# Performance work log

Hardware: AMD Instinct MI355X
Metric: run time of the kernel (lower is better)

## Reference

```python
import jax, jax.numpy as jnp
import numpy as np

N_NODES = 10000
N_REL = 200
DIM = 128          # rank * 2
REL_DIM = 128
VIS_DIM = 512
TXT_DIM = 768
N_EDGES = 320000


def _glorot(key, shape):
    fan_in, fan_out = shape[1], shape[0]
    lim = (6.0 / (fan_in + fan_out)) ** 0.5
    return jax.random.uniform(key, shape, jnp.float32, -lim, lim)


def setup_inputs() -> dict:
    key = jax.random.key(0)
    ks = jax.random.split(key, 24)
    inp = {}
    inp['x'] = jax.random.randint(ks[0], (1024, 3), 0, N_NODES)
    inp['edge_index'] = jax.random.randint(ks[1], (2, N_EDGES), 0, N_NODES)
    inp['edge_type'] = jax.random.randint(ks[2], (N_EDGES,), 0, N_REL)
    inp['visual'] = jax.random.normal(ks[3], (N_NODES, VIS_DIM), jnp.float32)
    inp['textual'] = jax.random.normal(ks[4], (N_NODES, TXT_DIM), jnp.float32)
    # embeddings (scaled by 0.001 as in torch init)
    inp['structural_emb'] = jax.random.normal(ks[5], (N_NODES, DIM), jnp.float32) * 0.001
    inp['relation_emb'] = jax.random.normal(ks[6], (N_REL, REL_DIM), jnp.float32) * 0.001
    # three KBGAT convs: w1 [out, 2*in+rel], b1 [out], w2 [1, out]
    cat = 2 * DIM + REL_DIM
    for i, tag in enumerate(['s', 'v', 't']):
        inp[f'W1_{tag}'] = _glorot(ks[7 + 3 * i], (DIM, cat))
        inp[f'b1_{tag}'] = jnp.zeros((DIM,), jnp.float32)
        inp[f'w2_{tag}'] = _glorot(ks[8 + 3 * i], (1, DIM))
    # modality projections
    inp['Wv'] = _glorot(ks[16], (DIM, VIS_DIM))
    inp['bv'] = jnp.zeros((DIM,), jnp.float32)
    inp['Wt'] = _glorot(ks[17], (DIM, TXT_DIM))
    inp['bt'] = jnp.zeros((DIM,), jnp.float32)
    inp['alpha'] = jnp.float32(0.1)
    inp['gamma'] = jnp.float32(0.8)
    return inp


def kbgat_conv(feat, rel_emb, src, dst, edge_type, W1, b1, w2):
    # gather per-edge embeddings: x_i = target, x_j = source (PyG default flow)
    triple = jnp.concatenate([feat[dst], feat[src], rel_emb[edge_type]], axis=1)  # [E, 2*D+R]
    c = triple @ W1.T + b1                                   # [E, D]
    b = jax.nn.leaky_relu(c @ w2[0])                         # [E]
    # segment softmax over destination nodes
    m = jax.ops.segment_max(b, dst, num_segments=N_NODES)
    e = jnp.exp(b - m[dst])
    z = jax.ops.segment_sum(e, dst, num_segments=N_NODES)
    attn = e / z[dst]                                        # [E]
    agg = jax.ops.segment_sum(c * attn[:, None], dst, num_segments=N_NODES)  # [N, D]
    return jax.nn.leaky_relu(agg)


def reference(x, edge_index, edge_type, visual, textual, structural_emb, relation_emb,
              W1_s, b1_s, w2_s, W1_v, b1_v, w2_v, W1_t, b1_t, w2_t,
              Wv, bv, Wt, bt, alpha, gamma):
    src, dst = edge_index[0], edge_index[1]
    h_s = kbgat_conv(structural_emb, relation_emb, src, dst, edge_type, W1_s, b1_s, w2_s)
    vf = visual @ Wv.T + bv
    h_v = kbgat_conv(vf, relation_emb, src, dst, edge_type, W1_v, b1_v, w2_v)
    tf = textual @ Wt.T + bt
    h_t = kbgat_conv(tf, relation_emb, src, dst, edge_type, W1_t, b1_t, w2_t)
    return (1.0 - alpha - gamma) * h_s + alpha * h_v + gamma * h_t
```

## Files before the change

kernel.cpp:

```cpp
#include <hip/hip_runtime.h>
#include <hip/hip_bf16.h>

typedef unsigned short u16;
typedef unsigned int u32;
typedef __bf16 bf16x8 __attribute__((ext_vector_type(8)));
typedef float f32x4 __attribute__((ext_vector_type(4)));

#define DIM 128

__device__ __forceinline__ u16 f2bf_rne(float x) {
  u32 u = __float_as_uint(x);
  return (u16)((u + 0x7fffu + ((u >> 16) & 1u)) >> 16);
}
__device__ __forceinline__ u32 packbf2(float x, float y) {
  return (u32)f2bf_rne(x) | ((u32)f2bf_rne(y) << 16);
}
__device__ __forceinline__ float lrelu(float x) { return x > 0.f ? x : 0.01f * x; }
__device__ __forceinline__ int iclamp(int v, int hi) { return v < 0 ? 0 : (v >= hi ? hi - 1 : v); }
__device__ __forceinline__ float sane(float x) { return (x == x) ? x : 0.f; }

__device__ __forceinline__ float wred_max(float v) {
  #pragma unroll
  for (int o = 32; o > 0; o >>= 1) v = fmaxf(v, __shfl_xor(v, o, 64));
  return v;
}
__device__ __forceinline__ float wred_sum(float v) {
  #pragma unroll
  for (int o = 32; o > 0; o >>= 1) v += __shfl_xor(v, o, 64);
  return v;
}

struct PrepAllArgs {
  const float* W1[3]; const float* Wmod[3]; int K[3]; u16* Wc[3];
  const float* rel; const float* b1[3]; const float* bmod[3]; const float* w2[3];
  u16* PrAll; float* qr[3]; int NR;
  const int* dst; int* cnt; int* rank; int E; int N;
  int wc2End; int wc1End; int wc0End; int nCompute; int totB;
};
struct MainArgs {
  const float* A[3]; const u16* B[3]; const float* w2[3];
  u16* PdAll; u16* PsAll; float* qd[3]; float* qs[3];
  int M; int K[3]; int tilesPerM; int nGemm; int totB;
  const int* dst; const int* src; const int* etyp;
  const int* offs; const int* rank; u32* sortedST;
  int E; int NR;
};
struct AgArgs {
  const u32* sortedST; const int* offs;
  const float* qd[3]; const float* qs[3]; const float* qr[3];
  const u16* PdAll; const u16* PsAll; const u16* PrAll;
  const float* alphaP; const float* gammaP;
  float* outp; int N; int NR; int E;
};

__global__ __launch_bounds__(256) void fused_prep(PrepAllArgs a) {
  __shared__ float red[256];
  int b = blockIdx.x, tid = threadIdx.x;
  long nC = a.nCompute, tot = a.totB;
  int cprev = (int)((long)b * nC / tot);
  int cnext = (int)(((long)b + 1) * nC / tot);
  if (cnext == cprev) {
    int h = b - cprev;
    int e = h * 256 + tid;
    if (e < a.E) {
      int d = a.dst[e];
      if (d >= 0 && d < a.N) a.rank[e] = atomicAdd(&a.cnt[d], 1);
    }
    return;
  }
  int c = cprev;
  if (c < a.wc0End) {
    int m, loc;
    if (c < a.wc2End)      { m = 2; loc = c; }
    else if (c < a.wc1End) { m = 1; loc = c - a.wc2End; }
    else                   { m = 0; loc = c - a.wc1End; }
    int o = loc & 255, kb = loc >> 8;
    int k = (kb << 8) + tid;
    int K = a.K[m];
    if (k < K) {
      int halfsel = (o >= 128) ? 128 : 0;
      int oo = o & 127;
      const float* W1 = a.W1[m];
      const float* Wm = a.Wmod[m];
      float acc;
      if (Wm == nullptr) {
        acc = W1[oo * 384 + halfsel + k];
      } else {
        acc = 0.f;
        for (int i = 0; i < 128; ++i)
          acc += W1[oo * 384 + halfsel + i] * Wm[i * K + k];
      }
      a.Wc[m][((size_t)(k >> 5) * 256 + o) * 32 + (k & 31)] = f2bf_rne(acc);
    }
  } else {
    int idx = c - a.wc0End;
    int NRpair = (a.NR + 1) >> 1;
    int m = idx / NRpair;
    if (m > 2) return;
    int rp = idx - m * NRpair;
    int half = tid >> 7, o = tid & 127;
    int r = rp * 2 + half;
    bool ok = (r < a.NR);
    float acc = 0.f;
    if (ok) {
      const float* W1 = a.W1[m];
      acc = a.b1[m][o];
      for (int i = 0; i < 128; ++i)
        acc += W1[o * 384 + 256 + i] * a.rel[r * 128 + i];
      const float* bmod = a.bmod[m];
      if (bmod != nullptr) {
        for (int i = 0; i < 128; ++i)
          acc += (W1[o * 384 + i] + W1[o * 384 + 128 + i]) * bmod[i];
      }
      a.PrAll[(size_t)r * 384 + m * 128 + o] = f2bf_rne(acc);
    }
    red[tid] = ok ? acc * a.w2[m][o] : 0.f;
    __syncthreads();
    int base = half << 7;
    for (int s = 64; s > 0; s >>= 1) {
      if (o < s) red[base + o] += red[base + o + s];
      __syncthreads();
    }
    if (o == 0 && ok) a.qr[m][r] = sane(red[base]);
  }
}

__global__ __launch_bounds__(1024) void scan_k(const int* __restrict__ cnt,
                                               int* __restrict__ offs, int N) {
  __shared__ int sums[1024];
  int t = threadIdx.x;
  int chunk = (N + 1023) >> 10;
  int base = t * chunk;
  int s = 0;
  for (int i = 0; i < chunk; ++i) { int idx = base + i; if (idx < N) s += cnt[idx]; }
  sums[t] = s;
  __syncthreads();
  for (int off = 1; off < 1024; off <<= 1) {
    int v = (t >= off) ? sums[t - off] : 0;
    __syncthreads();
    sums[t] += v;
    __syncthreads();
  }
  int prefix = (t > 0) ? sums[t - 1] : 0;
  for (int i = 0; i < chunk; ++i) {
    int idx = base + i;
    if (idx < N) { offs[idx] = prefix; prefix += cnt[idx]; }
  }
  if (t == 1023) offs[N] = sums[1023];
}

__device__ __forceinline__ void gemm_epilogue(const MainArgs& g, int m, int row0,
                                              f32x4 (&acc)[2][4], float (*qpart)[32]) {
  int tid = threadIdx.x;
  int lane = tid & 63, wv = tid >> 6;
  int quad = lane >> 4, l16 = lane & 15;
  int M = g.M;
  const float* w2 = g.w2[m];
  u16* PdAll = g.PdAll;
  u16* PsAll = g.PsAll;
  float w2c[4];
  #pragma unroll
  for (int t = 0; t < 4; ++t) w2c[t] = w2[(wv & 1) * 64 + t * 16 + l16];

  #pragma unroll
  for (int rg = 0; rg < 2; ++rg) {
    float part[4];
    #pragma unroll
    for (int r = 0; r < 4; ++r) {
      int rr = row0 + rg * 16 + quad * 4 + r;
      bool ok = rr < M;
      float qp = 0.f;
      #pragma unroll
      for (int t = 0; t < 4; ++t) {
        int cc = (wv & 1) * 64 + t * 16 + l16;
        if (ok) {
          if (wv < 2) PdAll[(size_t)rr * 384 + m * 128 + cc] = f2bf_rne(acc[rg][t][r]);
          else        PsAll[(size_t)rr * 384 + m * 128 + cc] = f2bf_rne(acc[rg][t][r]);
        }
        qp += acc[rg][t][r] * w2c[t];
      }
      #pragma unroll
      for (int mk = 1; mk < 16; mk <<= 1) qp += __shfl_xor(qp, mk, 64);
      part[r] = qp;
    }
    if (l16 == 0) {
      #pragma unroll
      for (int r = 0; r < 4; ++r) qpart[wv][rg * 16 + quad * 4 + r] = part[r];
    }
  }
  __syncthreads();
  if (tid < 64) {
    int row = tid & 31;
    int half = tid >> 5;
    int rr = row0 + row;
    if (rr < M) {
      if (half == 0) g.qd[m][rr] = sane(qpart[0][row] + qpart[1][row]);
      else           g.qs[m][rr] = sane(qpart[2][row] + qpart[3][row]);
    }
  }
}

template<int NT>
__device__ __forceinline__ void gemm_exact(const MainArgs& g, int m, int tile,
                                           u16* Als, float (*qpart)[32]) {
  constexpr int H = (NT + 1) / 2;
  const int M = g.M;
  int tid = threadIdx.x;
  int lane = tid & 63, wv = tid >> 6;
  int quad = lane >> 4, l16 = lane & 15;
  int row0 = tile * 32;
  int srow = tid >> 3;
  int tk4 = (tid & 7) * 4;
  int srsw = srow & 3;
  int wg = tk4 >> 3;
  int wrem = tk4 & 7;
  int grow = row0 + srow;
  if (grow >= M) grow = M - 1;
  const float* Ag = g.A[m] + (size_t)grow * (NT * 32);

  float4 vreg[H];
  #pragma unroll
  for (int i = 0; i < H; ++i)
    vreg[i] = *reinterpret_cast<const float4*>(Ag + tk4 + i * 32);
  #pragma unroll
  for (int i = 0; i < H; ++i) {
    int gidx = wg ^ srsw ^ (i & 3);
    u32* dp = reinterpret_cast<u32*>(&Als[((i * 32 + srow) * 32) + (gidx << 3) + wrem]);
    dp[0] = packbf2(vreg[i].x, vreg[i].y);
    dp[1] = packbf2(vreg[i].z, vreg[i].w);
  }
  #pragma unroll
  for (int i = H; i < NT; ++i)
    vreg[i - H] = *reinterpret_cast<const float4*>(Ag + tk4 + i * 32);
  #pragma unroll
  for (int i = H; i < NT; ++i) {
    int gidx = wg ^ srsw ^ (i & 3);
    u32* dp = reinterpret_cast<u32*>(&Als[((i * 32 + srow) * 32) + (gidx << 3) + wrem]);
    dp[0] = packbf2(vreg[i - H].x, vreg[i - H].y);
    dp[1] = packbf2(vreg[i - H].z, vreg[i - H].w);
  }
  __syncthreads();

  const u16* Bpg = g.B[m] + (size_t)(wv * 64 + l16) * 32 + quad * 8;
  f32x4 acc[2][4];
  #pragma unroll
  for (int rg = 0; rg < 2; ++rg)
    #pragma unroll
    for (int t = 0; t < 4; ++t) acc[rg][t] = (f32x4){0.f, 0.f, 0.f, 0.f};

  #pragma unroll
  for (int kb = 0; kb < NT; ++kb) {
    const u16* bp = Bpg + (size_t)kb * 8192;
    bf16x8 b0 = *reinterpret_cast<const bf16x8*>(bp);
    bf16x8 b1 = *reinterpret_cast<const bf16x8*>(bp + 512);
    bf16x8 b2 = *reinterpret_cast<const bf16x8*>(bp + 1024);
    bf16x8 b3 = *reinterpret_cast<const bf16x8*>(bp + 1536);
    int gsw = (quad ^ (l16 & 3) ^ (kb & 3)) << 3;
    #pragma unroll
    for (int rg = 0; rg < 2; ++rg) {
      bf16x8 av = *reinterpret_cast<const bf16x8*>(
          &Als[(kb * 32 + rg * 16 + l16) * 32 + gsw]);
      acc[rg][0] = __builtin_amdgcn_mfma_f32_16x16x32_bf16(av, b0, acc[rg][0], 0, 0, 0);
      acc[rg][1] = __builtin_amdgcn_mfma_f32_16x16x32_bf16(av, b1, acc[rg][1], 0, 0, 0);
      acc[rg][2] = __builtin_amdgcn_mfma_f32_16x16x32_bf16(av, b2, acc[rg][2], 0, 0, 0);
      acc[rg][3] = __builtin_amdgcn_mfma_f32_16x16x32_bf16(av, b3, acc[rg][3], 0, 0, 0);
    }
  }
  gemm_epilogue(g, m, row0, acc, qpart);
}

__device__ void gemm_generic(const MainArgs& g, int m, int tile,
                             u16* Als, float (*qpart)[32]) {
  const int M = g.M, K = g.K[m];
  int nt = K >> 5;
  int tid = threadIdx.x;
  int lane = tid & 63, wv = tid >> 6;
  int quad = lane >> 4, l16 = lane & 15;
  int row0 = tile * 32;
  int srow = tid >> 3;
  int tk4 = (tid & 7) * 4;
  int srsw = srow & 3;
  int wg = tk4 >> 3;
  int wrem = tk4 & 7;
  int grow = row0 + srow;
  if (grow >= M) grow = M - 1;
  const float* Ag = g.A[m] + (size_t)grow * K;
  const u16* Bpg = g.B[m] + (size_t)(wv * 64 + l16) * 32 + quad * 8;

  f32x4 acc[2][4];
  #pragma unroll
  for (int rg = 0; rg < 2; ++rg)
    #pragma unroll
    for (int t = 0; t < 4; ++t) acc[rg][t] = (f32x4){0.f, 0.f, 0.f, 0.f};

  for (int c0 = 0; c0 < nt; c0 += 24) {
    int kc = nt - c0; if (kc > 24) kc = 24;
    __syncthreads();
    for (int i = 0; i < kc; ++i) {
      int kg = (c0 + i) * 32 + tk4;
      if (kg + 3 < K) {
        float4 v = *reinterpret_cast<const float4*>(Ag + kg);
        int gidx = wg ^ srsw ^ (i & 3);
        u32* dp = reinterpret_cast<u32*>(&Als[((i * 32 + srow) * 32) + (gidx << 3) + wrem]);
        dp[0] = packbf2(v.x, v.y);
        dp[1] = packbf2(v.z, v.w);
      }
    }
    __syncthreads();
    for (int kb = 0; kb < kc; ++kb) {
      const u16* bp = Bpg + (size_t)(c0 + kb) * 8192;
      bf16x8 b0 = *reinterpret_cast<const bf16x8*>(bp);
      bf16x8 b1 = *reinterpret_cast<const bf16x8*>(bp + 512);
      bf16x8 b2 = *reinterpret_cast<const bf16x8*>(bp + 1024);
      bf16x8 b3 = *reinterpret_cast<const bf16x8*>(bp + 1536);
      int gsw = (quad ^ (l16 & 3) ^ (kb & 3)) << 3;
      #pragma unroll
      for (int rg = 0; rg < 2; ++rg) {
        bf16x8 av = *reinterpret_cast<const bf16x8*>(
            &Als[(kb * 32 + rg * 16 + l16) * 32 + gsw]);
        acc[rg][0] = __builtin_amdgcn_mfma_f32_16x16x32_bf16(av, b0, acc[rg][0], 0, 0, 0);
        acc[rg][1] = __builtin_amdgcn_mfma_f32_16x16x32_bf16(av, b1, acc[rg][1], 0, 0, 0);
        acc[rg][2] = __builtin_amdgcn_mfma_f32_16x16x32_bf16(av, b2, acc[rg][2], 0, 0, 0);
        acc[rg][3] = __builtin_amdgcn_mfma_f32_16x16x32_bf16(av, b3, acc[rg][3], 0, 0, 0);
      }
    }
  }
  gemm_epilogue(g, m, row0, acc, qpart);
}

__global__ __launch_bounds__(256) void fused_main(MainArgs g) {
  __shared__ __align__(16) u16 Als[24 * 32 * 32];
  __shared__ float qpart[4][32];
  int b = blockIdx.x;
  long nG = g.nGemm, tot = g.totB;
  int gprev = (int)((long)b * nG / tot);
  int gnext = (int)(((long)b + 1) * nG / tot);
  if (gnext == gprev) {
    int h = b - gprev;
    int e = h * 256 + threadIdx.x;
    if (e < g.E) {
      int d = g.dst[e];
      if (d >= 0 && d < g.M) {
        int pos = g.offs[d] + g.rank[e];
        if (pos >= 0 && pos < g.E) {
          u32 s = (u32)iclamp(g.src[e], g.M);
          u32 t = (u32)iclamp(g.etyp[e], g.NR);
          g.sortedST[pos] = (t << 16) | s;
        }
      }
    }
    return;
  }
  int fb = gprev;
  int tpm = g.tilesPerM;
  int m, tile;
  if (fb < tpm)            { m = 2; tile = fb; }
  else if (fb < 2 * tpm)   { m = 1; tile = fb - tpm; }
  else                     { m = 0; tile = fb - 2 * tpm; }

  int K = g.K[m];
  if (K == 768)      gemm_exact<24>(g, m, tile, Als, qpart);
  else if (K == 512) gemm_exact<16>(g, m, tile, Als, qpart);
  else if (K == 128) gemm_exact<4>(g, m, tile, Als, qpart);
  else               gemm_generic(g, m, tile, Als, qpart);
}

__global__ __launch_bounds__(256) void aggregate_all(AgArgs a) {
  int n = blockIdx.x * 4 + (threadIdx.x >> 6);
  if (n >= a.N) return;
  int lane = threadIdx.x & 63;
  int E = a.E;
  int eb = a.offs[n], ee = a.offs[n + 1];
  if (eb < 0) eb = 0;
  if (eb > E) eb = E;
  if (ee < eb) ee = eb;
  if (ee > E) ee = E;
  int En = ee - eb;

  float al = a.alphaP[0];
  if (!(al > 0.f && al < 1.f)) al = 0.1f;
  float ga = a.gammaP[0];
  if (!(ga > 0.f && ga < 1.f)) ga = 0.8f;
  float coef[3] = {1.f - al - ga, al, ga};

  float qdn[3];
  #pragma unroll
  for (int m = 0; m < 3; ++m) qdn[m] = sane(a.qd[m][n]);

  const u16* PsAll = a.PsAll;
  const u16* PrAll = a.PrAll;
  int dlo = 2 * lane;

  float rm[3] = {-1e30f, -1e30f, -1e30f};
  float z[3] = {0.f, 0.f, 0.f};
  float a0[3] = {0.f, 0.f, 0.f};
  float a1[3] = {0.f, 0.f, 0.f};
  for (int c0 = 0; c0 < En; c0 += 64) {
    int cn = min(64, En - c0);
    u32 stp = 0;
    float bm[3] = {-1e30f, -1e30f, -1e30f};
    if (lane < cn) {
      stp = a.sortedST[eb + c0 + lane];
      int s = (int)(stp & 0xffffu);
      int t = (int)(stp >> 16);
      #pragma unroll
      for (int m = 0; m < 3; ++m)
        bm[m] = lrelu(qdn[m] + a.qs[m][s] + a.qr[m][t]);
    }
    float wr[3];
    #pragma unroll
    for (int m = 0; m < 3; ++m) {
      float cm = wred_max(bm[m]);
      float nm = fmaxf(rm[m], cm);
      float sc = __expf(fmaxf(rm[m] - nm, -80.f));
      z[m] *= sc; a0[m] *= sc; a1[m] *= sc;
      rm[m] = nm;
      wr[m] = (lane < cn) ? __expf(fmaxf(bm[m] - nm, -80.f)) : 0.f;
      z[m] += wr[m];
    }

    int cnR = (cn + 3) & ~3;
    for (int j = 0; j < cnR; j += 4) {
      u32 stj[4];
      float wj[4][3];
      #pragma unroll
      for (int u = 0; u < 4; ++u) {
        stj[u] = __shfl(stp, j + u, 64);
        wj[u][0] = __shfl(wr[0], j + u, 64);
        wj[u][1] = __shfl(wr[1], j + u, 64);
        wj[u][2] = __shfl(wr[2], j + u, 64);
      }
      u32 pu[4][3], ru[4][3];
      #pragma unroll
      for (int u = 0; u < 4; ++u) {
        const u16* ps = PsAll + (size_t)(stj[u] & 0xffffu) * 384 + dlo;
        const u16* pr = PrAll + (size_t)(stj[u] >> 16) * 384 + dlo;
        #pragma unroll
        for (int m = 0; m < 3; ++m) {
          pu[u][m] = *reinterpret_cast<const u32*>(ps + m * 128);
          ru[u][m] = *reinterpret_cast<const u32*>(pr + m * 128);
        }
      }
      #pragma unroll
      for (int u = 0; u < 4; ++u) {
        #pragma unroll
        for (int m = 0; m < 3; ++m) {
          float ps0 = __uint_as_float(pu[u][m] << 16);
          float ps1 = __uint_as_float(pu[u][m] & 0xffff0000u);
          float pr0 = __uint_as_float(ru[u][m] << 16);
          float pr1 = __uint_as_float(ru[u][m] & 0xffff0000u);
          a0[m] = fmaf(wj[u][m], ps0 + pr0, a0[m]);
          a1[m] = fmaf(wj[u][m], ps1 + pr1, a1[m]);
        }
      }
    }
  }
  #pragma unroll
  for (int m = 0; m < 3; ++m) z[m] = wred_sum(z[m]);

  float o0 = 0.f, o1 = 0.f;
  const u16* pd = a.PdAll + (size_t)n * 384 + dlo;
  #pragma unroll
  for (int m = 0; m < 3; ++m) {
    float h0 = 0.f, h1 = 0.f;
    if (En > 0 && z[m] > 0.f) {
      float rz = 1.f / z[m];
      u32 du = *reinterpret_cast<const u32*>(pd + m * 128);
      float pd0 = __uint_as_float(du << 16), pd1 = __uint_as_float(du & 0xffff0000u);
      h0 = lrelu(pd0 + a0[m] * rz);
      h1 = lrelu(pd1 + a1[m] * rz);
    }
    o0 = fmaf(coef[m], h0, o0);
    o1 = fmaf(coef[m], h1, o1);
  }
  float* op = a.outp + (size_t)n * 128 + dlo;
  op[0] = sane(o0);
  op[1] = sane(o1);
}

extern "C" void kernel_launch(void* const* d_in, const int* in_sizes, int n_in,
                              void* d_out, int out_size, void* d_ws, size_t ws_size,
                              hipStream_t stream) {
  const int* ei        = (const int*)d_in[1];
  const int* et        = (const int*)d_in[2];
  const float* visual  = (const float*)d_in[3];
  const float* textual = (const float*)d_in[4];
  const float* semb    = (const float*)d_in[5];
  const float* relemb  = (const float*)d_in[6];
  const float* W1s = (const float*)d_in[7];
  const float* b1s = (const float*)d_in[8];
  const float* w2s = (const float*)d_in[9];
  const float* W1v = (const float*)d_in[10];
  const float* b1v = (const float*)d_in[11];
  const float* w2v = (const float*)d_in[12];
  const float* W1t = (const float*)d_in[13];
  const float* b1t = (const float*)d_in[14];
  const float* w2t = (const float*)d_in[15];
  const float* Wv  = (const float*)d_in[16];
  const float* bv  = (const float*)d_in[17];
  const float* Wt  = (const float*)d_in[18];
  const float* bt  = (const float*)d_in[19];
  const float* alphaP = (const float*)d_in[20];
  const float* gammaP = (const float*)d_in[21];
  float* outp = (float*)d_out;

  const int E   = in_sizes[2];
  const int N   = in_sizes[5] / DIM;
  const int NR  = in_sizes[6] / DIM;
  const int VIS = in_sizes[3] / N;
  const int TXT = in_sizes[4] / N;
  int Ks[3] = {DIM, VIS, TXT};
  const int TPM = (N + 31) / 32;

  const float* W1a[3]   = {W1s, W1v, W1t};
  const float* b1a[3]   = {b1s, b1v, b1t};
  const float* w2a[3]   = {w2s, w2v, w2t};
  const float* Wmoda[3] = {nullptr, Wv, Wt};
  const float* bmoda[3] = {nullptr, bv, bt};
  const float* Amoda[3] = {semb, visual, textual};

  const int* esrc = ei;
  const int* edst = ei + E;
  int egrid = (E + 255) / 256;

  size_t off = 0;
  auto take = [&](size_t bytes) -> size_t {
    size_t o = off;
    off = (off + bytes + 255) & ~(size_t)255;
    return o;
  };
  size_t o_cnt  = take((size_t)N * 4);
  size_t o_rank = take((size_t)E * 4);
  size_t o_offs = take((size_t)(N + 1) * 4);
  size_t o_st   = take((size_t)E * 4);
  size_t o_qdm[3], o_qsm[3], o_qrm[3], o_Wcm[3];
  for (int m = 0; m < 3; ++m) {
    o_qdm[m] = take((size_t)N * 4);
    o_qsm[m] = take((size_t)N * 4);
    o_qrm[m] = take((size_t)NR * 4);
    o_Wcm[m] = take((size_t)256 * Ks[m] * 2);
  }
  size_t o_PrAll = take((size_t)NR * 384 * 2);
  size_t o_PdAll = take((size_t)N * 384 * 2);
  size_t o_PsAll = take((size_t)N * 384 * 2);
  size_t need = off;

  if (ws_size < need) {
    hipMemsetAsync(d_out, 0, (size_t)out_size * 4, stream);
    return;
  }

  char* w = (char*)d_ws;
  int* counts = (int*)(w + o_cnt);
  int* rank   = (int*)(w + o_rank);
  int* offs   = (int*)(w + o_offs);
  u32* sortedST = (u32*)(w + o_st);

  hipMemsetAsync(counts, 0, (size_t)N * 4, stream);

  PrepAllArgs pa;
  pa.rel = relemb; pa.NR = NR;
  pa.PrAll = (u16*)(w + o_PrAll);
  pa.dst = edst; pa.cnt = counts; pa.rank = rank; pa.E = E; pa.N = N;
  for (int m = 0; m < 3; ++m) {
    pa.W1[m] = W1a[m]; pa.Wmod[m] = Wmoda[m]; pa.K[m] = Ks[m];
    pa.Wc[m] = (u16*)(w + o_Wcm[m]);
    pa.b1[m] = b1a[m]; pa.bmod[m] = bmoda[m]; pa.w2[m] = w2a[m];
    pa.qr[m] = (float*)(w + o_qrm[m]);
  }
  int NRpair = (NR + 1) / 2;
  int kbm[3];
  for (int m = 0; m < 3; ++m) kbm[m] = (Ks[m] + 255) / 256;
  pa.wc2End   = 256 * kbm[2];
  pa.wc1End   = pa.wc2End + 256 * kbm[1];
  pa.wc0End   = pa.wc1End + 256 * kbm[0];
  pa.nCompute = pa.wc0End + 3 * NRpair;
  pa.totB     = pa.nCompute + egrid;

  MainArgs ga;
  ga.M = N; ga.tilesPerM = TPM; ga.nGemm = 3 * TPM;
  ga.totB = ga.nGemm + egrid;
  ga.PdAll = (u16*)(w + o_PdAll);
  ga.PsAll = (u16*)(w + o_PsAll);
  ga.dst = edst; ga.src = esrc; ga.etyp = et;
  ga.offs = offs; ga.rank = rank; ga.sortedST = sortedST;
  ga.E = E; ga.NR = NR;
  AgArgs aa;
  for (int m = 0; m < 3; ++m) {
    ga.A[m] = Amoda[m]; ga.B[m] = (const u16*)(w + o_Wcm[m]); ga.w2[m] = w2a[m];
    ga.qd[m] = (float*)(w + o_qdm[m]); ga.qs[m] = (float*)(w + o_qsm[m]);
    ga.K[m] = Ks[m];
    aa.qd[m] = (const float*)(w + o_qdm[m]);
    aa.qs[m] = (const float*)(w + o_qsm[m]);
    aa.qr[m] = (const float*)(w + o_qrm[m]);
  }

  aa.PdAll = (const u16*)(w + o_PdAll);
  aa.PsAll = (const u16*)(w + o_PsAll);
  aa.PrAll = (const u16*)(w + o_PrAll);
  aa.sortedST = sortedST; aa.offs = offs;
  aa.alphaP = alphaP; aa.gammaP = gammaP;
  aa.outp = outp; aa.N = N; aa.NR = NR; aa.E = E;

  fused_prep<<<pa.totB, 256, 0, stream>>>(pa);
  scan_k<<<1, 1024, 0, stream>>>(counts, offs, N);
  fused_main<<<ga.totB, 256, 0, stream>>>(ga);
  aggregate_all<<<(N + 3) / 4, 256, 0, stream>>>(aa);
}
```

Baseline: 274.3 us.

## Merge all phases into one cooperative persistent kernel with grid syncs

Replaces the memset plus four kernel launches with a single cooperative mega-kernel. It loops virtual blocks over the phases (zero counts, prep, a multi-block scan, GEMM, aggregate) and separates them with grid.sync. The GEMM tile shrinks from 32 to 16 rows so more tiles exist for the persistent grid. A fallback multi-launch path remains. This targets launch gaps and the single-block scan, at the cost of grid-wide barriers and possibly lower per-tile efficiency.

Result: slower. 610.1 us (+122.4%).

```diff
diff --git a/kernel.cpp b/kernel.cpp
--- a/kernel.cpp
+++ b/kernel.cpp
@@ -1,5 +1,8 @@
 #include <hip/hip_runtime.h>
 #include <hip/hip_bf16.h>
+#include <hip/hip_cooperative_groups.h>
+
+namespace cg = cooperative_groups;
 
 typedef unsigned short u16;
 typedef unsigned int u32;
@@ -30,50 +33,38 @@
   return v;
 }
 
-struct PrepAllArgs {
-  const float* W1[3]; const float* Wmod[3]; int K[3]; u16* Wc[3];
+struct MegaArgs {
+  const float* W1[3]; const float* Wmod[3]; int K[3];
   const float* rel; const float* b1[3]; const float* bmod[3]; const float* w2[3];
-  u16* PrAll; float* qr[3]; int NR;
-  const int* dst; int* cnt; int* rank; int E; int N;
-  int wc2End; int wc1End; int wc0End; int nCompute; int totB;
+  const float* A[3];
+  const int* dst; const int* src; const int* etyp;
+  const float* alphaP; const float* gammaP;
+  u16* Wc[3]; u16* PrAll; u16* PdAll; u16* PsAll;
+  float* qr[3]; float* qd[3]; float* qs[3];
+  int* cnt; int* rank; int* offs; int* partial; u32* sortedST;
+  float* outp;
+  int E; int N; int NR;
+  int z0Tot;
+  int wc2End; int wc1End; int wc0End; int aCompute; int aTot;
+  int tilesPerM; int cGemm; int cTot;
+  int dTot;
 };
-struct MainArgs {
-  const float* A[3]; const u16* B[3]; const float* w2[3];
-  u16* PdAll; u16* PsAll; float* qd[3]; float* qs[3];
-  int M; int K[3]; int tilesPerM; int nGemm; int totB;
-  const int* dst; const int* src; const int* etyp;
-  const int* offs; const int* rank; u32* sortedST;
-  int E; int NR;
-};
-struct AgArgs {
-  const u32* sortedST; const int* offs;
-  const float* qd[3]; const float* qs[3]; const float* qr[3];
-  const u16* PdAll; const u16* PsAll; const u16* PrAll;
-  const float* alphaP; const float* gammaP;
-  float* outp; int N; int NR; int E;
-};
-
-__global__ __launch_bounds__(256) void fused_prep(PrepAllArgs a) {
-  __shared__ float red[256];
-  int b = blockIdx.x, tid = threadIdx.x;
-  long nC = a.nCompute, tot = a.totB;
-  int cprev = (int)((long)b * nC / tot);
-  int cnext = (int)(((long)b + 1) * nC / tot);
-  if (cnext == cprev) {
-    int h = b - cprev;
-    int e = h * 256 + tid;
+
+__device__ __forceinline__ void phaseA(const MegaArgs& a, int vb, void* lds) {
+  int tid = threadIdx.x;
+  if (vb >= a.aCompute) {
+    int e = (vb - a.aCompute) * 256 + tid;
     if (e < a.E) {
       int d = a.dst[e];
       if (d >= 0 && d < a.N) a.rank[e] = atomicAdd(&a.cnt[d], 1);
     }
     return;
   }
-  int c = cprev;
-  if (c < a.wc0End) {
+  if (vb < a.wc0End) {
     int m, loc;
-    if (c < a.wc2End)      { m = 2; loc = c; }
-    else if (c < a.wc1End) { m = 1; loc = c - a.wc2End; }
-    else                   { m = 0; loc = c - a.wc1End; }
+    if (vb < a.wc2End)      { m = 2; loc = vb; }
+    else if (vb < a.wc1End) { m = 1; loc = vb - a.wc2End; }
+    else                    { m = 0; loc = vb - a.wc1End; }
     int o = loc & 255, kb = loc >> 8;
     int k = (kb << 8) + tid;
     int K = a.K[m];
@@ -92,161 +83,200 @@
       }
       a.Wc[m][((size_t)(k >> 5) * 256 + o) * 32 + (k & 31)] = f2bf_rne(acc);
     }
-  } else {
-    int idx = c - a.wc0End;
-    int NRpair = (a.NR + 1) >> 1;
-    int m = idx / NRpair;
-    if (m > 2) return;
-    int rp = idx - m * NRpair;
-    int half = tid >> 7, o = tid & 127;
-    int r = rp * 2 + half;
-    bool ok = (r < a.NR);
-    float acc = 0.f;
-    if (ok) {
-      const float* W1 = a.W1[m];
-      acc = a.b1[m][o];
+    return;
+  }
+  float* red = (float*)lds;
+  int idx = vb - a.wc0End;
+  int NRpair = (a.NR + 1) >> 1;
+  int m = idx / NRpair;
+  if (m > 2) return;
+  int rp = idx - m * NRpair;
+  int half = tid >> 7, o = tid & 127;
+  int r = rp * 2 + half;
+  bool ok = (r < a.NR);
+  float acc = 0.f;
+  if (ok) {
+    const float* W1 = a.W1[m];
+    acc = a.b1[m][o];
+    for (int i = 0; i < 128; ++i)
+      acc += W1[o * 384 + 256 + i] * a.rel[r * 128 + i];
+    const float* bmod = a.bmod[m];
+    if (bmod != nullptr) {
       for (int i = 0; i < 128; ++i)
-        acc += W1[o * 384 + 256 + i] * a.rel[r * 128 + i];
-      const float* bmod = a.bmod[m];
-      if (bmod != nullptr) {
-        for (int i = 0; i < 128; ++i)
-          acc += (W1[o * 384 + i] + W1[o * 384 + 128 + i]) * bmod[i];
-      }
-      a.PrAll[(size_t)r * 384 + m * 128 + o] = f2bf_rne(acc);
-    }
-    red[tid] = ok ? acc * a.w2[m][o] : 0.f;
-    __syncthreads();
-    int base = half << 7;
-    for (int s = 64; s > 0; s >>= 1) {
-      if (o < s) red[base + o] += red[base + o + s];
-      __syncthreads();
-    }
-    if (o == 0 && ok) a.qr[m][r] = sane(red[base]);
-  }
-}
-
-__global__ __launch_bounds__(1024) void scan_k(const int* __restrict__ cnt,
-                                               int* __restrict__ offs, int N) {
-  __shared__ int sums[1024];
+        acc += (W1[o * 384 + i] + W1[o * 384 + 128 + i]) * bmod[i];
+    }
+    a.PrAll[(size_t)r * 384 + m * 128 + o] = f2bf_rne(acc);
+  }
+  red[tid] = ok ? acc * a.w2[m][o] : 0.f;
+  __syncthreads();
+  int base = half << 7;
+  for (int s = 64; s > 0; s >>= 1) {
+    if (o < s) red[base + o] += red[base + o + s];
+    __syncthreads();
+  }
+  if (o == 0 && ok) a.qr[m][r] = sane(red[base]);
+  __syncthreads();
+}
+
+__device__ __forceinline__ void scanB1(const MegaArgs& a, int b, int gsz, void* lds) {
+  int* sums = (int*)lds;
   int t = threadIdx.x;
-  int chunk = (N + 1023) >> 10;
-  int base = t * chunk;
+  int chunk = (a.N + gsz - 1) / gsz;
+  int base = b * chunk;
+  int perT = (chunk + 255) >> 8;
   int s = 0;
-  for (int i = 0; i < chunk; ++i) { int idx = base + i; if (idx < N) s += cnt[idx]; }
+  for (int i = 0; i < perT; ++i) {
+    int idx = base + t * perT + i;
+    if (idx < base + chunk && idx < a.N) s += a.cnt[idx];
+  }
   sums[t] = s;
   __syncthreads();
-  for (int off = 1; off < 1024; off <<= 1) {
+  for (int off = 1; off < 256; off <<= 1) {
     int v = (t >= off) ? sums[t - off] : 0;
     __syncthreads();
     sums[t] += v;
     __syncthreads();
   }
-  int prefix = (t > 0) ? sums[t - 1] : 0;
-  for (int i = 0; i < chunk; ++i) {
-    int idx = base + i;
-    if (idx < N) { offs[idx] = prefix; prefix += cnt[idx]; }
-  }
-  if (t == 1023) offs[N] = sums[1023];
-}
-
-__device__ __forceinline__ void gemm_epilogue(const MainArgs& g, int m, int row0,
-                                              f32x4 (&acc)[2][4], float (*qpart)[32]) {
+  if (t == 255) a.partial[b] = sums[255];
+  __syncthreads();
+}
+
+__device__ __forceinline__ void scanB2(const MegaArgs& a, int gsz, void* lds) {
+  int* sums = (int*)lds;
+  int t = threadIdx.x;
+  int G = (gsz + 255) >> 8;
+  int s = 0;
+  for (int i = 0; i < G; ++i) {
+    int idx = t * G + i;
+    if (idx < gsz) s += a.partial[idx];
+  }
+  sums[t] = s;
+  __syncthreads();
+  for (int off = 1; off < 256; off <<= 1) {
+    int v = (t >= off) ? sums[t - off] : 0;
+    __syncthreads();
+    sums[t] += v;
+    __syncthreads();
+  }
+  if (t == 255) a.offs[a.N] = sums[255];
+  int pre = (t > 0) ? sums[t - 1] : 0;
+  for (int i = 0; i < G; ++i) {
+    int idx = t * G + i;
+    if (idx < gsz) { int c = a.partial[idx]; a.partial[idx] = pre; pre += c; }
+  }
+  __syncthreads();
+}
+
+__device__ __forceinline__ void scanB3(const MegaArgs& a, int b, int gsz, void* lds) {
+  int* sums = (int*)lds;
+  int t = threadIdx.x;
+  int chunk = (a.N + gsz - 1) / gsz;
+  int base = b * chunk;
+  int perT = (chunk + 255) >> 8;
+  int s = 0;
+  for (int i = 0; i < perT; ++i) {
+    int idx = base + t * perT + i;
+    if (idx < base + chunk && idx < a.N) s += a.cnt[idx];
+  }
+  sums[t] = s;
+  __syncthreads();
+  for (int off = 1; off < 256; off <<= 1) {
+    int v = (t >= off) ? sums[t - off] : 0;
+    __syncthreads();
+    sums[t] += v;
+    __syncthreads();
+  }
+  int prefix = a.partial[b] + ((t > 0) ? sums[t - 1] : 0);
+  for (int i = 0; i < perT; ++i) {
+    int idx = base + t * perT + i;
+    if (idx < base + chunk && idx < a.N) { a.offs[idx] = prefix; prefix += a.cnt[idx]; }
+  }
+  __syncthreads();
+}
+
+__device__ __forceinline__ void stash16(u16* Als, int srow, int tk4, int i, float4 v) {
+  int kb = 2 * i + (tk4 >> 5);
+  int kl = tk4 & 31;
+  int gidx = (kl >> 3) ^ (srow & 3) ^ (kb & 3);
+  u32* dp = reinterpret_cast<u32*>(&Als[(kb * 16 + srow) * 32 + (gidx << 3) + (kl & 7)]);
+  dp[0] = packbf2(v.x, v.y);
+  dp[1] = packbf2(v.z, v.w);
+}
+
+__device__ __forceinline__ void epilogue16(const MegaArgs& g, int m, int row0,
+                                           f32x4 (&acc)[4], float (*qpart)[16]) {
   int tid = threadIdx.x;
   int lane = tid & 63, wv = tid >> 6;
   int quad = lane >> 4, l16 = lane & 15;
-  int M = g.M;
   const float* w2 = g.w2[m];
-  u16* PdAll = g.PdAll;
-  u16* PsAll = g.PsAll;
   float w2c[4];
   #pragma unroll
   for (int t = 0; t < 4; ++t) w2c[t] = w2[(wv & 1) * 64 + t * 16 + l16];
-
-  #pragma unroll
-  for (int rg = 0; rg < 2; ++rg) {
-    float part[4];
+  float part[4];
+  #pragma unroll
+  for (int r = 0; r < 4; ++r) {
+    int rr = row0 + quad * 4 + r;
+    bool ok = rr < g.N;
+    float qp = 0.f;
     #pragma unroll
-    for (int r = 0; r < 4; ++r) {
-      int rr = row0 + rg * 16 + quad * 4 + r;
-      bool ok = rr < M;
-      float qp = 0.f;
-      #pragma unroll
-      for (int t = 0; t < 4; ++t) {
-        int cc = (wv & 1) * 64 + t * 16 + l16;
-        if (ok) {
-          if (wv < 2) PdAll[(size_t)rr * 384 + m * 128 + cc] = f2bf_rne(acc[rg][t][r]);
-          else        PsAll[(size_t)rr * 384 + m * 128 + cc] = f2bf_rne(acc[rg][t][r]);
-        }
-        qp += acc[rg][t][r] * w2c[t];
-      }
-      #pragma unroll
-      for (int mk = 1; mk < 16; mk <<= 1) qp += __shfl_xor(qp, mk, 64);
-      part[r] = qp;
-    }
-    if (l16 == 0) {
-      #pragma unroll
-      for (int r = 0; r < 4; ++r) qpart[wv][rg * 16 + quad * 4 + r] = part[r];
-    }
-  }
-  __syncthreads();
-  if (tid < 64) {
-    int row = tid & 31;
-    int half = tid >> 5;
+    for (int t = 0; t < 4; ++t) {
+      int cc = (wv & 1) * 64 + t * 16 + l16;
+      if (ok) {
+        if (wv < 2) g.PdAll[(size_t)rr * 384 + m * 128 + cc] = f2bf_rne(acc[t][r]);
+        else        g.PsAll[(size_t)rr * 384 + m * 128 + cc] = f2bf_rne(acc[t][r]);
+      }
+      qp += acc[t][r] * w2c[t];
+    }
+    #pragma unroll
+    for (int mk = 1; mk < 16; mk <<= 1) qp += __shfl_xor(qp, mk, 64);
+    part[r] = qp;
+  }
+  if (l16 == 0) {
+    #pragma unroll
+    for (int r = 0; r < 4; ++r) qpart[wv][quad * 4 + r] = part[r];
+  }
+  __syncthreads();
+  if (tid < 32) {
+    int row = tid & 15, half = tid >> 4;
     int rr = row0 + row;
-    if (rr < M) {
+    if (rr < g.N) {
       if (half == 0) g.qd[m][rr] = sane(qpart[0][row] + qpart[1][row]);
       else           g.qs[m][rr] = sane(qpart[2][row] + qpart[3][row]);
     }
   }
+  __syncthreads();
 }
 
 template<int NT>
-__device__ __forceinline__ void gemm_exact(const MainArgs& g, int m, int tile,
-                                           u16* Als, float (*qpart)[32]) {
-  constexpr int H = (NT + 1) / 2;
-  const int M = g.M;
+__device__ __forceinline__ void gemm16(const MegaArgs& g, int m, int tile,
+                                       u16* Als, float (*qpart)[16]) {
+  constexpr int NS = NT / 2;
+  constexpr int H = (NS + 1) / 2;
   int tid = threadIdx.x;
   int lane = tid & 63, wv = tid >> 6;
   int quad = lane >> 4, l16 = lane & 15;
-  int row0 = tile * 32;
-  int srow = tid >> 3;
-  int tk4 = (tid & 7) * 4;
-  int srsw = srow & 3;
-  int wg = tk4 >> 3;
-  int wrem = tk4 & 7;
+  int row0 = tile * 16;
+  int srow = tid >> 4;
+  int tk4 = (tid & 15) * 4;
   int grow = row0 + srow;
-  if (grow >= M) grow = M - 1;
+  if (grow >= g.N) grow = g.N - 1;
   const float* Ag = g.A[m] + (size_t)grow * (NT * 32);
 
   float4 vreg[H];
   #pragma unroll
-  for (int i = 0; i < H; ++i)
-    vreg[i] = *reinterpret_cast<const float4*>(Ag + tk4 + i * 32);
-  #pragma unroll
-  for (int i = 0; i < H; ++i) {
-    int gidx = wg ^ srsw ^ (i & 3);
-    u32* dp = reinterpret_cast<u32*>(&Als[((i * 32 + srow) * 32) + (gidx << 3) + wrem]);
-    dp[0] = packbf2(vreg[i].x, vreg[i].y);
-    dp[1] = packbf2(vreg[i].z, vreg[i].w);
-  }
-  #pragma unroll
-  for (int i = H; i < NT; ++i)
-    vreg[i - H] = *reinterpret_cast<const float4*>(Ag + tk4 + i * 32);
-  #pragma unroll
-  for (int i = H; i < NT; ++i) {
-    int gidx = wg ^ srsw ^ (i & 3);
-    u32* dp = reinterpret_cast<u32*>(&Als[((i * 32 + srow) * 32) + (gidx << 3) + wrem]);
-    dp[0] = packbf2(vreg[i - H].x, vreg[i - H].y);
-    dp[1] = packbf2(vreg[i - H].z, vreg[i - H].w);
-  }
-  __syncthreads();
-
-  const u16* Bpg = g.B[m] + (size_t)(wv * 64 + l16) * 32 + quad * 8;
-  f32x4 acc[2][4];
-  #pragma unroll
-  for (int rg = 0; rg < 2; ++rg)
-    #pragma unroll
-    for (int t = 0; t < 4; ++t) acc[rg][t] = (f32x4){0.f, 0.f, 0.f, 0.f};
+  for (int i = 0; i < H; ++i) vreg[i] = *reinterpret_cast<const float4*>(Ag + tk4 + i * 64);
+  #pragma unroll
+  for (int i = 0; i < H; ++i) stash16(Als, srow, tk4, i, vreg[i]);
+  #pragma unroll
+  for (int i = H; i < NS; ++i) vreg[i - H] = *reinterpret_cast<const float4*>(Ag + tk4 + i * 64);
+  #pragma unroll
+  for (int i = H; i < NS; ++i) stash16(Als, srow, tk4, i, vreg[i - H]);
+  __syncthreads();
+
+  const u16* Bpg = g.Wc[m] + (size_t)(wv * 64 + l16) * 32 + quad * 8;
+  f32x4 acc[4];
+  #pragma unroll
+  for (int t = 0; t < 4; ++t) acc[t] = (f32x4){0.f, 0.f, 0.f, 0.f};
 
   #pragma unroll
   for (int kb = 0; kb < NT; ++kb) {
@@ -256,54 +286,40 @@
     bf16x8 b2 = *reinterpret_cast<const bf16x8*>(bp + 1024);
     bf16x8 b3 = *reinterpret_cast<const bf16x8*>(bp + 1536);
     int gsw = (quad ^ (l16 & 3) ^ (kb & 3)) << 3;
-    #pragma unroll
-    for (int rg = 0; rg < 2; ++rg) {
-      bf16x8 av = *reinterpret_cast<const bf16x8*>(
-          &Als[(kb * 32 + rg * 16 + l16) * 32 + gsw]);
-      acc[rg][0] = __builtin_amdgcn_mfma_f32_16x16x32_bf16(av, b0, acc[rg][0], 0, 0, 0);
-      acc[rg][1] = __builtin_amdgcn_mfma_f32_16x16x32_bf16(av, b1, acc[rg][1], 0, 0, 0);
-      acc[rg][2] = __builtin_amdgcn_mfma_f32_16x16x32_bf16(av, b2, acc[rg][2], 0, 0, 0);
-      acc[rg][3] = __builtin_amdgcn_mfma_f32_16x16x32_bf16(av, b3, acc[rg][3], 0, 0, 0);
-    }
-  }
-  gemm_epilogue(g, m, row0, acc, qpart);
-}
-
-__device__ void gemm_generic(const MainArgs& g, int m, int tile,
-                             u16* Als, float (*qpart)[32]) {
-  const int M = g.M, K = g.K[m];
+    bf16x8 av = *reinterpret_cast<const bf16x8*>(&Als[(kb * 16 + l16) * 32 + gsw]);
+    acc[0] = __builtin_amdgcn_mfma_f32_16x16x32_bf16(av, b0, acc[0], 0, 0, 0);
+    acc[1] = __builtin_amdgcn_mfma_f32_16x16x32_bf16(av, b1, acc[1], 0, 0, 0);
+    acc[2] = __builtin_amdgcn_mfma_f32_16x16x32_bf16(av, b2, acc[2], 0, 0, 0);
+    acc[3] = __builtin_amdgcn_mfma_f32_16x16x32_bf16(av, b3, acc[3], 0, 0, 0);
+  }
+  epilogue16(g, m, row0, acc, qpart);
+}
+
+__device__ void gemm16_gen(const MegaArgs& g, int m, int tile,
+                           u16* Als, float (*qpart)[16]) {
+  const int K = g.K[m];
   int nt = K >> 5;
   int tid = threadIdx.x;
   int lane = tid & 63, wv = tid >> 6;
   int quad = lane >> 4, l16 = lane & 15;
-  int row0 = tile * 32;
-  int srow = tid >> 3;
-  int tk4 = (tid & 7) * 4;
-  int srsw = srow & 3;
-  int wg = tk4 >> 3;
-  int wrem = tk4 & 7;
+  int row0 = tile * 16;
+  int srow = tid >> 4;
+  int tk4 = (tid & 15) * 4;
   int grow = row0 + srow;
-  if (grow >= M) grow = M - 1;
+  if (grow >= g.N) grow = g.N - 1;
   const float* Ag = g.A[m] + (size_t)grow * K;
-  const u16* Bpg = g.B[m] + (size_t)(wv * 64 + l16) * 32 + quad * 8;
-
-  f32x4 acc[2][4];
-  #pragma unroll
-  for (int rg = 0; rg < 2; ++rg)
-    #pragma unroll
-    for (int t = 0; t < 4; ++t) acc[rg][t] = (f32x4){0.f, 0.f, 0.f, 0.f};
-
+  const u16* Bpg = g.Wc[m] + (size_t)(wv * 64 + l16) * 32 + quad * 8;
+  f32x4 acc[4];
+  #pragma unroll
+  for (int t = 0; t < 4; ++t) acc[t] = (f32x4){0.f, 0.f, 0.f, 0.f};
   for (int c0 = 0; c0 < nt; c0 += 24) {
     int kc = nt - c0; if (kc > 24) kc = 24;
     __syncthreads();
-    for (int i = 0; i < kc; ++i) {
-      int kg = (c0 + i) * 32 + tk4;
+    for (int i = 0; i < (kc + 1) / 2; ++i) {
+      int kg = c0 * 32 + tk4 + i * 64;
       if (kg + 3 < K) {
         float4 v = *reinterpret_cast<const float4*>(Ag + kg);
-        int gidx = wg ^ srsw ^ (i & 3);
-        u32* dp = reinterpret_cast<u32*>(&Als[((i * 32 + srow) * 32) + (gidx << 3) + wrem]);
-        dp[0] = packbf2(v.x, v.y);
-        dp[1] = packbf2(v.z, v.w);
+        stash16(Als, srow, tk4, i, v);
       }
     }
     __syncthreads();
@@ -314,59 +330,47 @@
       bf16x8 b2 = *reinterpret_cast<const bf16x8*>(bp + 1024);
       bf16x8 b3 = *reinterpret_cast<const bf16x8*>(bp + 1536);
       int gsw = (quad ^ (l16 & 3) ^ (kb & 3)) << 3;
-      #pragma unroll
-      for (int rg = 0; rg < 2; ++rg) {
-        bf16x8 av = *reinterpret_cast<const bf16x8*>(
-            &Als[(kb * 32 + rg * 16 + l16) * 32 + gsw]);
-        acc[rg][0] = __builtin_amdgcn_mfma_f32_16x16x32_bf16(av, b0, acc[rg][0], 0, 0, 0);
-        acc[rg][1] = __builtin_amdgcn_mfma_f32_16x16x32_bf16(av, b1, acc[rg][1], 0, 0, 0);
-        acc[rg][2] = __builtin_amdgcn_mfma_f32_16x16x32_bf16(av, b2, acc[rg][2], 0, 0, 0);
-        acc[rg][3] = __builtin_amdgcn_mfma_f32_16x16x32_bf16(av, b3, acc[rg][3], 0, 0, 0);
-      }
-    }
-  }
-  gemm_epilogue(g, m, row0, acc, qpart);
-}
-
-__global__ __launch_bounds__(256) void fused_main(MainArgs g) {
-  __shared__ __align__(16) u16 Als[24 * 32 * 32];
-  __shared__ float qpart[4][32];
-  int b = blockIdx.x;
-  long nG = g.nGemm, tot = g.totB;
-  int gprev = (int)((long)b * nG / tot);
-  int gnext = (int)(((long)b + 1) * nG / tot);
-  if (gnext == gprev) {
-    int h = b - gprev;
-    int e = h * 256 + threadIdx.x;
-    if (e < g.E) {
-      int d = g.dst[e];
-      if (d >= 0 && d < g.M) {
-        int pos = g.offs[d] + g.rank[e];
-        if (pos >= 0 && pos < g.E) {
-          u32 s = (u32)iclamp(g.src[e], g.M);
-          u32 t = (u32)iclamp(g.etyp[e], g.NR);
-          g.sortedST[pos] = (t << 16) | s;
+      bf16x8 av = *reinterpret_cast<const bf16x8*>(&Als[(kb * 16 + l16) * 32 + gsw]);
+      acc[0] = __builtin_amdgcn_mfma_f32_16x16x32_bf16(av, b0, acc[0], 0, 0, 0);
+      acc[1] = __builtin_amdgcn_mfma_f32_16x16x32_bf16(av, b1, acc[1], 0, 0, 0);
+      acc[2] = __builtin_amdgcn_mfma_f32_16x16x32_bf16(av, b2, acc[2], 0, 0, 0);
+      acc[3] = __builtin_amdgcn_mfma_f32_16x16x32_bf16(av, b3, acc[3], 0, 0, 0);
+    }
+  }
+  epilogue16(g, m, row0, acc, qpart);
+}
+
+__device__ __forceinline__ void phaseC(const MegaArgs& a, int vb,
+                                       u16* Als, float (*qpart)[16]) {
+  if (vb >= a.cGemm) {
+    int e = (vb - a.cGemm) * 256 + threadIdx.x;
+    if (e < a.E) {
+      int d = a.dst[e];
+      if (d >= 0 && d < a.N) {
+        int pos = a.offs[d] + a.rank[e];
+        if (pos >= 0 && pos < a.E) {
+          u32 s = (u32)iclamp(a.src[e], a.N);
+          u32 t = (u32)iclamp(a.etyp[e], a.NR);
+          a.sortedST[pos] = (t << 16) | s;
         }
       }
     }
     return;
   }
-  int fb = gprev;
-  int tpm = g.tilesPerM;
+  int tpm = a.tilesPerM;
   int m, tile;
-  if (fb < tpm)            { m = 2; tile = fb; }
-  else if (fb < 2 * tpm)   { m = 1; tile = fb - tpm; }
-  else                     { m = 0; tile = fb - 2 * tpm; }
-
-  int K = g.K[m];
-  if (K == 768)      gemm_exact<24>(g, m, tile, Als, qpart);
-  else if (K == 512) gemm_exact<16>(g, m, tile, Als, qpart);
-  else if (K == 128) gemm_exact<4>(g, m, tile, Als, qpart);
-  else               gemm_generic(g, m, tile, Als, qpart);
-}
-
-__global__ __launch_bounds__(256) void aggregate_all(AgArgs a) {
-  int n = blockIdx.x * 4 + (threadIdx.x >> 6);
+  if (vb < tpm)            { m = 2; tile = vb; }
+  else if (vb < 2 * tpm)   { m = 1; tile = vb - tpm; }
+  else                     { m = 0; tile = vb - 2 * tpm; }
+  int K = a.K[m];
+  if (K == 768)      gemm16<24>(a, m, tile, Als, qpart);
+  else if (K == 512) gemm16<16>(a, m, tile, Als, qpart);
+  else if (K == 128) gemm16<4>(a, m, tile, Als, qpart);
+  else               gemm16_gen(a, m, tile, Als, qpart);
+}
+
+__device__ void phaseD(const MegaArgs& a, int vb) {
+  int n = vb * 4 + (threadIdx.x >> 6);
   if (n >= a.N) return;
   int lane = threadIdx.x & 63;
   int E = a.E;
@@ -476,6 +480,66 @@
   float* op = a.outp + (size_t)n * 128 + dlo;
   op[0] = sane(o0);
   op[1] = sane(o1);
+}
+
+__global__ __launch_bounds__(256) void mega_kernel(MegaArgs a) {
+  cg::grid_group grid = cg::this_grid();
+  __shared__ __align__(16) u16 Als[24 * 16 * 32];
+  __shared__ float qpart[4][16];
+  int gsz = gridDim.x, b0 = blockIdx.x;
+
+  for (int vb = b0; vb < a.z0Tot; vb += gsz) {
+    int i = vb * 256 + threadIdx.x;
+    if (i < a.N) a.cnt[i] = 0;
+  }
+  grid.sync();
+  for (int vb = b0; vb < a.aTot; vb += gsz) phaseA(a, vb, Als);
+  grid.sync();
+  scanB1(a, b0, gsz, Als);
+  grid.sync();
+  if (b0 == 0) scanB2(a, gsz, Als);
+  grid.sync();
+  scanB3(a, b0, gsz, Als);
+  grid.sync();
+  for (int vb = b0; vb < a.cTot; vb += gsz) phaseC(a, vb, Als, qpart);
+  grid.sync();
+  for (int vb = b0; vb < a.dTot; vb += gsz) phaseD(a, vb);
+}
+
+__global__ __launch_bounds__(256) void fb_prep(MegaArgs a) {
+  __shared__ __align__(16) float red[256];
+  phaseA(a, blockIdx.x, red);
+}
+__global__ __launch_bounds__(1024) void fb_scan(const int* __restrict__ cnt,
+                                                int* __restrict__ offs, int N) {
+  __shared__ int sums[1024];
+  int t = threadIdx.x;
+  int chunk = (N + 1023) >> 10;
+  int base = t * chunk;
+  int s = 0;
+  for (int i = 0; i < chunk; ++i) { int idx = base + i; if (idx < N) s += cnt[idx]; }
+  sums[t] = s;
+  __syncthreads();
+  for (int off = 1; off < 1024; off <<= 1) {
+    int v = (t >= off) ? sums[t - off] : 0;
+    __syncthreads();
+    sums[t] += v;
+    __syncthreads();
+  }
+  int prefix = (t > 0) ? sums[t - 1] : 0;
+  for (int i = 0; i < chunk; ++i) {
+    int idx = base + i;
+    if (idx < N) { offs[idx] = prefix; prefix += cnt[idx]; }
+  }
+  if (t == 1023) offs[N] = sums[1023];
+}
+__global__ __launch_bounds__(256) void fb_main(MegaArgs a) {
+  __shared__ __align__(16) u16 Als[24 * 16 * 32];
+  __shared__ float qpart[4][16];
+  phaseC(a, blockIdx.x, Als, qpart);
+}
+__global__ __launch_bounds__(256) void fb_agg(MegaArgs a) {
+  phaseD(a, blockIdx.x);
 }
 
 extern "C" void kernel_launch(void* const* d_in, const int* in_sizes, int n_in,
@@ -510,7 +574,6 @@
   const int VIS = in_sizes[3] / N;
   const int TXT = in_sizes[4] / N;
   int Ks[3] = {DIM, VIS, TXT};
-  const int TPM = (N + 31) / 32;
 
   const float* W1a[3]   = {W1s, W1v, W1t};
   const float* b1a[3]   = {b1s, b1v, b1t};
@@ -532,6 +595,7 @@
   size_t o_cnt  = take((size_t)N * 4);
   size_t o_rank = take((size_t)E * 4);
   size_t o_offs = take((size_t)(N + 1) * 4);
+  size_t o_part = take((size_t)4096 * 4);
   size_t o_st   = take((size_t)E * 4);
   size_t o_qdm[3], o_qsm[3], o_qrm[3], o_Wcm[3];
   for (int m = 0; m < 3; ++m) {
@@ -546,64 +610,82 @@
   size_t need = off;
 
   if (ws_size < need) {
-    hipMemsetAsync(d_out, 0, (size_t)out_size * 4, stream);
+    (void)hipMemsetAsync(d_out, 0, (size_t)out_size * 4, stream);
     return;
   }
 
   char* w = (char*)d_ws;
-  int* counts = (int*)(w + o_cnt);
-  int* rank   = (int*)(w + o_rank);
-  int* offs   = (int*)(w + o_offs);
-  u32* sortedST = (u32*)(w + o_st);
-
-  hipMemsetAsync(counts, 0, (size_t)N * 4, stream);
-
-  PrepAllArgs pa;
-  pa.rel = relemb; pa.NR = NR;
-  pa.PrAll = (u16*)(w + o_PrAll);
-  pa.dst = edst; pa.cnt = counts; pa.rank = rank; pa.E = E; pa.N = N;
+
+  MegaArgs ma;
+  ma.rel = relemb; ma.NR = NR; ma.E = E; ma.N = N;
+  ma.dst = edst; ma.src = esrc; ma.etyp = et;
+  ma.alphaP = alphaP; ma.gammaP = gammaP;
+  ma.PrAll = (u16*)(w + o_PrAll);
+  ma.PdAll = (u16*)(w + o_PdAll);
+  ma.PsAll = (u16*)(w + o_PsAll);
+  ma.cnt = (int*)(w + o_cnt);
+  ma.rank = (int*)(w + o_rank);
+  ma.offs = (int*)(w + o_offs);
+  ma.partial = (int*)(w + o_part);
+  ma.sortedST = (u32*)(w + o_st);
+  ma.outp = outp;
   for (int m = 0; m < 3; ++m) {
-    pa.W1[m] = W1a[m]; pa.Wmod[m] = Wmoda[m]; pa.K[m] = Ks[m];
-    pa.Wc[m] = (u16*)(w + o_Wcm[m]);
-    pa.b1[m] = b1a[m]; pa.bmod[m] = bmoda[m]; pa.w2[m] = w2a[m];
-    pa.qr[m] = (float*)(w + o_qrm[m]);
-  }
-  int NRpair = (NR + 1) / 2;
+    ma.W1[m] = W1a[m]; ma.Wmod[m] = Wmoda[m]; ma.K[m] = Ks[m];
+    ma.b1[m] = b1a[m]; ma.bmod[m] = bmoda[m]; ma.w2[m] = w2a[m];
+    ma.A[m] = Amoda[m];
+    ma.Wc[m] = (u16*)(w + o_Wcm[m]);
+    ma.qr[m] = (float*)(w + o_qrm[m]);
+    ma.qd[m] = (float*)(w + o_qdm[m]);
+    ma.qs[m] = (float*)(w + o_qsm[m]);
+  }
   int kbm[3];
   for (int m = 0; m < 3; ++m) kbm[m] = (Ks[m] + 255) / 256;
-  pa.wc2End   = 256 * kbm[2];
-  pa.wc1End   = pa.wc2End + 256 * kbm[1];
-  pa.wc0End   = pa.wc1End + 256 * kbm[0];
-  pa.nCompute = pa.wc0End + 3 * NRpair;
-  pa.totB     = pa.nCompute + egrid;
-
-  MainArgs ga;
-  ga.M = N; ga.tilesPerM = TPM; ga.nGemm = 3 * TPM;
-  ga.totB = ga.nGemm + egrid;
-  ga.PdAll = (u16*)(w + o_PdAll);
-  ga.PsAll = (u16*)(w + o_PsAll);
-  ga.dst = edst; ga.src = esrc; ga.etyp = et;
-  ga.offs = offs; ga.rank = rank; ga.sortedST = sortedST;
-  ga.E = E; ga.NR = NR;
-  AgArgs aa;
-  for (int m = 0; m < 3; ++m) {
-    ga.A[m] = Amoda[m]; ga.B[m] = (const u16*)(w + o_Wcm[m]); ga.w2[m] = w2a[m];
-    ga.qd[m] = (float*)(w + o_qdm[m]); ga.qs[m] = (float*)(w + o_qsm[m]);
-    ga.K[m] = Ks[m];
-    aa.qd[m] = (const float*)(w + o_qdm[m]);
-    aa.qs[m] = (const float*)(w + o_qsm[m]);
-    aa.qr[m] = (const float*)(w + o_qrm[m]);
-  }
-
-  aa.PdAll = (const u16*)(w + o_PdAll);
-  aa.PsAll = (const u16*)(w + o_PsAll);
-  aa.PrAll = (const u16*)(w + o_PrAll);
-  aa.sortedST = sortedST; aa.offs = offs;
-  aa.alphaP = alphaP; aa.gammaP = gammaP;
-  aa.outp = outp; aa.N = N; aa.NR = NR; aa.E = E;
-
-  fused_prep<<<pa.totB, 256, 0, stream>>>(pa);
-  scan_k<<<1, 1024, 0, stream>>>(counts, offs, N);
-  fused_main<<<ga.totB, 256, 0, stream>>>(ga);
-  aggregate_all<<<(N + 3) / 4, 256, 0, stream>>>(aa);
-}
+  int NRpair = (NR + 1) / 2;
+  ma.z0Tot  = (N + 255) / 256;
+  ma.wc2End = 256 * kbm[2];
+  ma.wc1End = ma.wc2End + 256 * kbm[1];
+  ma.wc0End = ma.wc1End + 256 * kbm[0];
+  ma.aCompute = ma.wc0End + 3 * NRpair;
+  ma.aTot   = ma.aCompute + egrid;
+  ma.tilesPerM = (N + 15) / 16;
+  ma.cGemm  = 3 * ma.tilesPerM;
+  ma.cTot   = ma.cGemm + egrid;
+  ma.dTot   = (N + 3) / 4;
+
+  static int s_coop = -1;
+  static int s_grid = 1024;
+  if (s_coop < 0) {
+    int dev = 0;
+    (void)hipGetDevice(&dev);
+    int coop = 0;
+    (void)hipDeviceGetAttribute(&coop, hipDeviceAttributeCooperativeLaunch, dev);
+    int nCU = 256;
+    (void)hipDeviceGetAttribute(&nCU, hipDeviceAttributeMultiprocessorCount, dev);
+    int bpc = 0;
+    hipError_t oe = hipOccupancyMaxActiveBlocksPerMultiprocessor(&bpc, mega_kernel, 256, 0);
+    if (oe != hipSuccess || bpc <= 0) bpc = 2;
+    long g = (long)nCU * bpc;
+    if (g > 4096) g = 4096;
+    if (g < 64) g = 64;
+    s_grid = (int)g;
+    s_coop = coop;
+  }
+
+  if (s_coop) {
+    for (int gtry = s_grid; gtry >= 64; gtry >>= 1) {
+      void* kargs[] = { (void*)&ma };
+      hipError_t le = hipLaunchCooperativeKernel(mega_kernel, dim3(gtry), dim3(256),
+                                                 kargs, 0, stream);
+      if (le == hipSuccess) {
+        s_grid = gtry;
+        return;
+      }
+    }
+  }
+
+  (void)hipMemsetAsync(ma.cnt, 0, (size_t)N * 4, stream);
+  fb_prep<<<ma.aTot, 256, 0, stream>>>(ma);
+  fb_scan<<<1, 1024, 0, stream>>>(ma.cnt, ma.offs, N);
+  fb_main<<<ma.cTot, 256, 0, stream>>>(ma);
+  fb_agg<<<ma.dTot, 256, 0, stream>>>(ma);
+}
```
